# Optimization experiments

Measured on AMD Instinct MI355X. Metric: run time of the kernel, lower is better.

The kernel has to match this reference:

```python
import jax, jax.numpy as jnp
import numpy as np

D_MODEL = 128
D_STATE = 16
D_CONV = 2
EXPAND = 2
D_INNER = EXPAND * D_MODEL  # 256
DT_RANK = (D_MODEL + 15) // 16  # 8
GROUPS = 4
EPS = 1e-5


def setup_inputs() -> dict:
    key = jax.random.key(0)
    ks = jax.random.split(key, 12)
    s = lambda k, shape, sc=0.02: jax.random.normal(k, shape, dtype=jnp.float32) * sc
    inp = {
        "x_hsi": jax.random.normal(ks[0], (8, D_MODEL, 64, 64), dtype=jnp.float32),
        "W_in": s(ks[1], (D_MODEL, 2 * D_INNER)),            # in_proj (no bias)
        "conv_w": s(ks[2], (D_INNER, D_CONV), 0.5),          # depthwise causal conv, k=2
        "conv_b": s(ks[3], (D_INNER,), 0.1),
        "W_x": s(ks[4], (D_INNER, DT_RANK + 2 * D_STATE)),   # x_proj (no bias)
        "W_dt": s(ks[5], (DT_RANK, D_INNER), 0.1),
        "b_dt": s(ks[6], (D_INNER,), 0.1),
        "A_log": jnp.log(jnp.broadcast_to(jnp.arange(1, D_STATE + 1, dtype=jnp.float32), (D_INNER, D_STATE))),
        "D": jnp.ones((D_INNER,), dtype=jnp.float32),
        "W_out": s(ks[7], (D_INNER, D_MODEL)),               # out_proj (no bias)
        "gn_gamma": jnp.ones((D_MODEL,), dtype=jnp.float32),
        "gn_beta": jnp.zeros((D_MODEL,), dtype=jnp.float32),
    }
    return inp


def _causal_conv_k2(x, w, b):
    # x: [B, L, Din]; w: [Din, 2]; causal depthwise conv, kernel size 2
    xp = jnp.pad(x, ((0, 0), (1, 0), (0, 0)))
    return xp[:, :-1] * w[:, 0] + xp[:, 1:] * w[:, 1] + b


def _selective_scan(xc, dt, Bmat, Cmat, A, D):
    # xc,dt: [B,L,Din]; Bmat,Cmat: [B,L,N]; A: [Din,N]; D: [Din]
    def step(h, inp):
        dt_t, B_t, C_t, x_t = inp          # [B,Din],[B,N],[B,N],[B,Din]
        dA = jnp.exp(dt_t[..., None] * A)                      # [B,Din,N]
        dBx = dt_t[..., None] * B_t[:, None, :] * x_t[..., None]
        h = dA * h + dBx
        y = jnp.einsum('bdn,bn->bd', h, C_t)
        return h, y

    B_, L, Din = xc.shape
    h0 = jnp.zeros((B_, Din, A.shape[1]), dtype=xc.dtype)
    xs = (jnp.swapaxes(dt, 0, 1), jnp.swapaxes(Bmat, 0, 1),
          jnp.swapaxes(Cmat, 0, 1), jnp.swapaxes(xc, 0, 1))
    _, ys = jax.lax.scan(step, h0, xs)     # ys: [L,B,Din]
    return jnp.swapaxes(ys, 0, 1) + xc * D


def _mamba(x, W_in, conv_w, conv_b, W_x, W_dt, b_dt, A_log, D, W_out):
    # x: [B, L, d_model]
    xz = x @ W_in                                   # [B,L,2*Din]
    xh, z = jnp.split(xz, 2, axis=-1)
    xh = jax.nn.silu(_causal_conv_k2(xh, conv_w, conv_b))
    x_dbl = xh @ W_x                                # [B,L,dt_rank+2N]
    dt_low = x_dbl[..., :DT_RANK]
    Bmat = x_dbl[..., DT_RANK:DT_RANK + D_STATE]
    Cmat = x_dbl[..., DT_RANK + D_STATE:]
    dt = jax.nn.softplus(dt_low @ W_dt + b_dt)      # [B,L,Din]
    A = -jnp.exp(A_log)
    y = _selective_scan(xh, dt, Bmat, Cmat, A, D)
    y = y * jax.nn.silu(z)
    return y @ W_out


def _group_norm(x, gamma, beta):
    # x: [B,C,H,W]
    B_, C, H, W = x.shape
    xr = x.reshape(B_, GROUPS, -1)
    mean = xr.mean(-1, keepdims=True)
    var = xr.var(-1, keepdims=True)
    xn = ((xr - mean) * jax.lax.rsqrt(var + EPS)).reshape(B_, C, H, W)
    return xn * gamma[:, None, None] + beta[:, None, None]


def reference(x_hsi, W_in, conv_w, conv_b, W_x, W_dt, b_dt, A_log, D, W_out, gn_gamma, gn_beta):
    B_, C, H, W = x_hsi.shape
    x = jnp.transpose(x_hsi, (0, 2, 3, 1)).reshape(B_, H * W, C)
    x = _mamba(x, W_in, conv_w, conv_b, W_x, W_dt, b_dt, A_log, D, W_out)
    x = jnp.transpose(x.reshape(B_, H, W, C), (0, 3, 1, 2))
    x = jax.nn.silu(_group_norm(x, gn_gamma, gn_beta))
    return x + x_hsi
```

## Files before the change

kernel.cpp:

```cpp
#include <hip/hip_runtime.h>
#include <hip/hip_bf16.h>
#include <hip/hip_fp16.h>
#include <math.h>

#define BATCH   8
#define LSEQ    4096
#define CMODEL  128
#define DIN     256
#define NSTATE  16
#define RRANK   8
#define NCH     128
#define TCH     32

typedef __attribute__((ext_vector_type(8))) short short8;
typedef __attribute__((ext_vector_type(4))) float f32x4;
typedef __attribute__((ext_vector_type(2))) float f32x2;

__device__ __forceinline__ float sigmoid_fast(float x) {
    return __builtin_amdgcn_rcpf(1.0f + __expf(-x));
}
__device__ __forceinline__ float silu_fast(float x) { return x * sigmoid_fast(x); }
__device__ __forceinline__ float softplus_fast(float x) {
    return fmaxf(x, 0.0f) + __logf(1.0f + __expf(-fabsf(x)));
}
__device__ __forceinline__ float bf2f(unsigned short u) {
    return __uint_as_float(((unsigned)u) << 16);
}
__device__ __forceinline__ unsigned pk2bf(float a, float b) {
    __hip_bfloat162 t = __float22bfloat162_rn(make_float2(a, b));
    unsigned r;
    __builtin_memcpy(&r, &t, 4);
    return r;
}
__device__ __forceinline__ unsigned short f2bf1(float v) {
    return (unsigned short)pk2bf(v, v);
}
__device__ __forceinline__ f32x2 up2(unsigned w) {
    return (f32x2){ __uint_as_float(w << 16), __uint_as_float(w & 0xffff0000u) };
}

__device__ __forceinline__ void dA_powers2(float dtv, const float* A, bool fast,
                                           f32x2* dA2)
{
    if (fast) {
        float e1 = __expf(dtv * A[0]);
        float e2 = e1 * e1;
        dA2[0] = (f32x2){e1, e2};
        f32x2 e2s = (f32x2){e2, e2};
        #pragma unroll
        for (int j = 1; j < 8; ++j) dA2[j] = dA2[j-1] * e2s;
    } else {
        #pragma unroll
        for (int j = 0; j < 8; ++j)
            dA2[j] = (f32x2){__expf(dtv * A[2*j]), __expf(dtv * A[2*j+1])};
    }
}

#define LSTR 72

__device__ __forceinline__ void tr64_bf(const float* __restrict__ src, int lds,
                                        int r0, int c0,
                                        unsigned short* __restrict__ dst, int ldd)
{
    __shared__ float ts[64][65];
    const int tid = threadIdx.x;
    #pragma unroll
    for (int it = 0; it < 4; ++it) {
        int slot = tid + it * 256;
        int i = slot >> 4, j4 = slot & 15;
        float4 v = *(const float4*)&src[(size_t)(r0 + i) * lds + c0 + j4 * 4];
        ts[i][j4*4+0] = v.x; ts[i][j4*4+1] = v.y;
        ts[i][j4*4+2] = v.z; ts[i][j4*4+3] = v.w;
    }
    __syncthreads();
    #pragma unroll
    for (int it = 0; it < 4; ++it) {
        int slot = tid + it * 256;
        int row = slot >> 4, c4 = slot & 15;
        unsigned p0 = pk2bf(ts[c4*4+0][row], ts[c4*4+1][row]);
        unsigned p1 = pk2bf(ts[c4*4+2][row], ts[c4*4+3][row]);
        unsigned long long u = (unsigned long long)p0 | ((unsigned long long)p1 << 32);
        *(unsigned long long*)&dst[(size_t)(c0 + row) * ldd + r0 + c4 * 4] = u;
    }
}

__global__ __launch_bounds__(256) void k0_setup(
    const float* __restrict__ W_in, const float* __restrict__ W_out,
    unsigned short* __restrict__ wtin, unsigned short* __restrict__ wtout,
    float* __restrict__ part)
{
    const int bid = blockIdx.x;
    if (bid < 16) {
        int ct = bid >> 3, jt = bid & 7;
        tr64_bf(W_in, 512, ct * 64, jt * 64, wtin, 128);
    } else if (bid < 24) {
        int t3 = bid - 16;
        int kt = t3 >> 1, ct = t3 & 1;
        tr64_bf(W_out, 128, kt * 64, ct * 64, wtout, 256);
    } else {
        if (threadIdx.x < 64) part[threadIdx.x] = 0.0f;
    }
}

__global__ __launch_bounds__(512) void k1_gemm_in(
    const float* __restrict__ x_hsi, const unsigned short* __restrict__ wtin,
    unsigned short* __restrict__ xhbf, unsigned short* __restrict__ zbf)
{
    __shared__ __align__(16) unsigned short Abf[128 * LSTR];
    __shared__ __align__(16) unsigned short Bbf[256 * LSTR];
    const int tid = threadIdx.x;
    const int R0  = blockIdx.x * 128;
    const int b   = R0 >> 12;
    const int l0  = R0 & 4095;
    const int jbase = blockIdx.y * 256;

    const int w    = tid >> 6;
    const int lane = tid & 63;
    const int lm   = lane & 15;
    const int q    = lane >> 4;
    const int mbase = (w & 1) * 64;
    const int nbase = (w >> 1) * 64;

    f32x4 acc[4][4];
    #pragma unroll
    for (int i = 0; i < 4; ++i)
        #pragma unroll
        for (int j = 0; j < 4; ++j) acc[i][j] = (f32x4){0.f, 0.f, 0.f, 0.f};

    const int cq = tid & 15;
    const int lq = tid >> 4;

    for (int kc = 0; kc < 128; kc += 64) {
        __syncthreads();
        {
            float v[4][4];
            #pragma unroll
            for (int t = 0; t < 4; ++t) {
                float4 f = *(const float4*)&x_hsi[((b * 128 + kc + cq * 4 + t) << 12) + l0 + lq * 4];
                v[t][0] = f.x; v[t][1] = f.y; v[t][2] = f.z; v[t][3] = f.w;
            }
            #pragma unroll
            for (int i = 0; i < 4; ++i) {
                unsigned p0 = pk2bf(v[0][i], v[1][i]);
                unsigned p1 = pk2bf(v[2][i], v[3][i]);
                unsigned long long u = (unsigned long long)p0 | ((unsigned long long)p1 << 32);
                *(unsigned long long*)&Abf[(lq * 4 + i) * LSTR + cq * 4] = u;
            }
        }
        #pragma unroll
        for (int it = 0; it < 4; ++it) {
            int slot = tid + it * 512;
            int r = slot >> 3, seg = slot & 7;
            short8 vb = *(const short8*)&wtin[(size_t)(jbase + r) * 128 + kc + seg * 8];
            *(short8*)&Bbf[r * LSTR + seg * 8] = vb;
        }
        __syncthreads();
        #pragma unroll
        for (int kt = 0; kt < 2; ++kt) {
            short8 af[4], bfr[4];
            #pragma unroll
            for (int mt = 0; mt < 4; ++mt)
                af[mt] = *(const short8*)&Abf[(mbase + mt * 16 + lm) * LSTR + kt * 32 + q * 8];
            #pragma unroll
            for (int nt = 0; nt < 4; ++nt)
                bfr[nt] = *(const short8*)&Bbf[(nbase + nt * 16 + lm) * LSTR + kt * 32 + q * 8];
            #pragma unroll
            for (int mt = 0; mt < 4; ++mt)
                #pragma unroll
                for (int nt = 0; nt < 4; ++nt)
                    acc[mt][nt] = __builtin_amdgcn_mfma_f32_16x16x32_bf16(
                        af[mt], bfr[nt], acc[mt][nt], 0, 0, 0);
        }
    }

    const bool is_xh = (jbase == 0);
    #pragma unroll
    for (int mt = 0; mt < 4; ++mt) {
        #pragma unroll
        for (int r = 0; r < 4; ++r) {
            int row = R0 + mbase + mt * 16 + q * 4 + r;
            #pragma unroll
            for (int nt = 0; nt < 4; ++nt) {
                int col = nbase + nt * 16 + lm;
                float val = acc[mt][nt][r];
                if (is_xh) xhbf[row * 256 + col] = f2bf1(val);
                else       zbf[row * 256 + col]  = f2bf1(silu_fast(val));
            }
        }
    }
}

__global__ __launch_bounds__(256) void k4_xdbl(
    const unsigned short* __restrict__ xhbf, const float* __restrict__ conv_w,
    const float* __restrict__ conv_b, const float* __restrict__ W_x,
    float* __restrict__ xdbl, unsigned short* __restrict__ xcbf)
{
    __shared__ float xcs[128][68];
    __shared__ float wxs[64 * 40];
    __shared__ float cw0[256], cw1[256], cbs[256];
    const int tid = threadIdx.x;
    cw0[tid] = conv_w[2 * tid];
    cw1[tid] = conv_w[2 * tid + 1];
    cbs[tid] = conv_b[tid];

    const int R0 = blockIdx.x * 128;
    const int tc = tid & 7;
    const int tr = tid >> 3;

    float acc[4][5];
    #pragma unroll
    for (int i = 0; i < 4; ++i)
        #pragma unroll
        for (int j = 0; j < 5; ++j) acc[i][j] = 0.0f;

    for (int kc = 0; kc < 256; kc += 64) {
        __syncthreads();
        #pragma unroll
        for (int it = 0; it < 3; ++it) {
            int i4 = tid + it * 256;
            if (i4 < 640) ((float4*)wxs)[i4] = ((const float4*)&W_x[kc * 40])[i4];
        }
        #pragma unroll
        for (int it = 0; it < 8; ++it) {
            int idx = tid + it * 256;
            int r = idx >> 4, qq = idx & 15;
            int row = R0 + r;
            ushort4 cu = *(const ushort4*)&xhbf[(size_t)row * 256 + kc + qq * 4];
            float cur[4] = {bf2f(cu.x), bf2f(cu.y), bf2f(cu.z), bf2f(cu.w)};
            float pv[4] = {0.f, 0.f, 0.f, 0.f};
            if ((row & 4095) != 0) {
                ushort4 pu = *(const ushort4*)&xhbf[(size_t)(row - 1) * 256 + kc + qq * 4];
                pv[0] = bf2f(pu.x); pv[1] = bf2f(pu.y);
                pv[2] = bf2f(pu.z); pv[3] = bf2f(pu.w);
            }
            int d = kc + qq * 4;
            float o[4];
            #pragma unroll
            for (int e = 0; e < 4; ++e)
                o[e] = silu_fast(pv[e] * cw0[d+e] + cur[e] * cw1[d+e] + cbs[d+e]);
            *(float4*)&xcs[r][qq * 4] = make_float4(o[0], o[1], o[2], o[3]);
            unsigned p0 = pk2bf(o[0], o[1]), p1 = pk2bf(o[2], o[3]);
            unsigned long long u = (unsigned long long)p0 | ((unsigned long long)p1 << 32);
            *(unsigned long long*)&xcbf[(size_t)row * 256 + d] = u;
        }
        __syncthreads();
        #pragma unroll 2
        for (int k = 0; k < 64; ++k) {
            float wv[5];
            #pragma unroll
            for (int j = 0; j < 5; ++j) wv[j] = wxs[k * 40 + tc * 5 + j];
            #pragma unroll
            for (int i = 0; i < 4; ++i) {
                float a = xcs[tr * 4 + i][k];
                #pragma unroll
                for (int j = 0; j < 5; ++j) acc[i][j] = fmaf(a, wv[j], acc[i][j]);
            }
        }
    }
    #pragma unroll
    for (int i = 0; i < 4; ++i) {
        int row = R0 + tr * 4 + i;
        #pragma unroll
        for (int j = 0; j < 5; ++j) xdbl[row * 40 + tc * 5 + j] = acc[i][j];
    }
}

__global__ __launch_bounds__(256) void k6_scan1(
    const unsigned short* __restrict__ xcbf, const float* __restrict__ xdbl,
    const float* __restrict__ W_dt, const float* __restrict__ b_dt,
    const float* __restrict__ A_log,
    float* __restrict__ hend, float* __restrict__ dtsg,
    __half* __restrict__ dtvh)
{
    __shared__ __align__(16) unsigned char xdb[TCH * 64];
    const int d = threadIdx.x;
    const int chunk = blockIdx.x;
    const int b = blockIdx.y;
    const int t0 = b * LSEQ + chunk * TCH;

    {
        int row = d >> 3, seg = d & 7;
        const float4* src = (const float4*)&xdbl[(size_t)(t0 + row) * 40];
        if (seg < 2) {
            *(float4*)&xdb[row * 64 + seg * 16] = src[seg];
        } else if (seg < 6) {
            float4 f = src[seg];
            unsigned p0 = pk2bf(f.x, f.y), p1 = pk2bf(f.z, f.w);
            *(uint2*)&xdb[row * 64 + 32 + (seg - 2) * 8] = make_uint2(p0, p1);
        }
    }

    float A[16];
    #pragma unroll
    for (int qq = 0; qq < 4; ++qq) {
        float4 al = *(const float4*)&A_log[d * 16 + qq * 4];
        A[qq*4+0] = -__expf(al.x); A[qq*4+1] = -__expf(al.y);
        A[qq*4+2] = -__expf(al.z); A[qq*4+3] = -__expf(al.w);
    }
    bool fast = true;
    #pragma unroll
    for (int n = 1; n < 16; ++n)
        fast = fast && (fabsf(A[n] - (n + 1) * A[0]) <= 1e-4f * fabsf(A[n]) + 1e-7f);

    float wdt[8];
    #pragma unroll
    for (int r = 0; r < 8; ++r) wdt[r] = W_dt[r * 256 + d];
    const float bdt = b_dt[d];

    f32x2 h2[8];
    #pragma unroll
    for (int j = 0; j < 8; ++j) h2[j] = (f32x2){0.f, 0.f};
    float dtsum = 0.f;
    __syncthreads();

    #pragma unroll 2
    for (int tt = 0; tt < TCH; ++tt) {
        const int row = t0 + tt;
        float xcv = bf2f(xcbf[(size_t)row * 256 + d]);

        const unsigned char* xr = &xdb[tt * 64];
        float dl[8];
        *(float4*)&dl[0] = *(const float4*)xr;
        *(float4*)&dl[4] = *(const float4*)(xr + 16);
        float dtr = bdt;
        #pragma unroll
        for (int r = 0; r < 8; ++r) dtr = fmaf(dl[r], wdt[r], dtr);
        float dtv = softplus_fast(dtr);
        dtsum += dtv;
        float dtx = dtv * xcv;
        dtvh[(size_t)row * 256 + d] = __float2half(dtv);

        uint4 bu0 = *(const uint4*)(xr + 32);
        uint4 bu1 = *(const uint4*)(xr + 48);
        f32x2 Bt2[8] = {up2(bu0.x), up2(bu0.y), up2(bu0.z), up2(bu0.w),
                        up2(bu1.x), up2(bu1.y), up2(bu1.z), up2(bu1.w)};

        f32x2 dA2[8];
        dA_powers2(dtv, A, fast, dA2);
        f32x2 dtx2 = (f32x2){dtx, dtx};
        #pragma unroll
        for (int j = 0; j < 8; ++j)
            h2[j] = dA2[j] * h2[j] + dtx2 * Bt2[j];
    }

    const float* hf = (const float*)h2;
    const int base = ((b * NCH + chunk) * 256 + d) * 16;
    #pragma unroll
    for (int qq = 0; qq < 4; ++qq)
        *(float4*)&hend[base + qq * 4] = make_float4(hf[qq*4], hf[qq*4+1], hf[qq*4+2], hf[qq*4+3]);
    dtsg[(b * NCH + chunk) * 256 + d] = dtsum;
}

__global__ __launch_bounds__(256) void k7_combine(
    const float* __restrict__ dtsg, const float* __restrict__ A_log,
    float* __restrict__ hx)
{
    const int idx = blockIdx.x * 256 + threadIdx.x;
    const int b = idx >> 12;
    const int rem = idx & 4095;
    const int d = rem >> 4, n = rem & 15;
    const float An = -__expf(A_log[d * 16 + n]);
    const int base = b * NCH * 4096 + rem;
    const int sbase = b * NCH * 256 + d;
    float h = 0.f;
    float Sb[8], Eb[8];
    #pragma unroll
    for (int j = 0; j < 8; ++j) {
        Sb[j] = dtsg[sbase + j * 256];
        Eb[j] = hx[base + j * 4096];
    }
    for (int g = 0; g < NCH / 8; ++g) {
        const int o  = base + g * 32768;
        const int so = sbase + g * 2048;
        float Sn[8] = {0,0,0,0,0,0,0,0}, En[8] = {0,0,0,0,0,0,0,0};
        if (g < NCH / 8 - 1) {
            #pragma unroll
            for (int j = 0; j < 8; ++j) {
                Sn[j] = dtsg[so + 2048 + j * 256];
                En[j] = hx[o + 32768 + j * 4096];
            }
        }
        #pragma unroll
        for (int j = 0; j < 8; ++j) {
            hx[o + j * 4096] = h;
            float P = __expf(Sb[j] * An);
            h = fmaf(P, h, Eb[j]);
        }
        #pragma unroll
        for (int j = 0; j < 8; ++j) { Sb[j] = Sn[j]; Eb[j] = En[j]; }
    }
}

__global__ __launch_bounds__(256) void k8_scan2(
    const unsigned short* __restrict__ xcbf, const float* __restrict__ xdbl,
    const __half* __restrict__ dtvh, const float* __restrict__ A_log,
    const float* __restrict__ Dvec, const float* __restrict__ hin,
    const unsigned short* __restrict__ zbf, unsigned short* __restrict__ ybf)
{
    __shared__ __align__(16) unsigned char xdb[TCH * 64];
    const int d = threadIdx.x;
    const int chunk = blockIdx.x;
    const int b = blockIdx.y;
    const int t0 = b * LSEQ + chunk * TCH;

    {
        int row = d >> 3, seg = d & 7;
        float4 f = *(const float4*)&xdbl[(size_t)(t0 + row) * 40 + 8 + seg * 4];
        unsigned p0 = pk2bf(f.x, f.y), p1 = pk2bf(f.z, f.w);
        *(uint2*)&xdb[row * 64 + seg * 8] = make_uint2(p0, p1);
    }

    float A[16];
    #pragma unroll
    for (int qq = 0; qq < 4; ++qq) {
        float4 al = *(const float4*)&A_log[d * 16 + qq * 4];
        A[qq*4+0] = -__expf(al.x); A[qq*4+1] = -__expf(al.y);
        A[qq*4+2] = -__expf(al.z); A[qq*4+3] = -__expf(al.w);
    }
    bool fast = true;
    #pragma unroll
    for (int n = 1; n < 16; ++n)
        fast = fast && (fabsf(A[n] - (n + 1) * A[0]) <= 1e-4f * fabsf(A[n]) + 1e-7f);

    const float Dd = Dvec[d];

    f32x2 h2[8];
    const int hbase = ((b * NCH + chunk) * 256 + d) * 16;
    {
        float hf[16];
        #pragma unroll
        for (int qq = 0; qq < 4; ++qq) {
            float4 hv = *(const float4*)&hin[hbase + qq * 4];
            hf[qq*4+0] = hv.x; hf[qq*4+1] = hv.y; hf[qq*4+2] = hv.z; hf[qq*4+3] = hv.w;
        }
        #pragma unroll
        for (int j = 0; j < 8; ++j) h2[j] = (f32x2){hf[2*j], hf[2*j+1]};
    }
    __syncthreads();

    #pragma unroll 2
    for (int tt = 0; tt < TCH; ++tt) {
        const int row = t0 + tt;
        const size_t gi = (size_t)row * 256 + d;
        float dtv = __half2float(dtvh[gi]);
        float xcv = bf2f(xcbf[gi]);
        float dtx = dtv * xcv;

        const unsigned char* xr = &xdb[tt * 64];
        uint4 bu0 = *(const uint4*)(xr + 0);
        uint4 bu1 = *(const uint4*)(xr + 16);
        uint4 cu0 = *(const uint4*)(xr + 32);
        uint4 cu1 = *(const uint4*)(xr + 48);
        f32x2 Bt2[8] = {up2(bu0.x), up2(bu0.y), up2(bu0.z), up2(bu0.w),
                        up2(bu1.x), up2(bu1.y), up2(bu1.z), up2(bu1.w)};
        f32x2 Ct2[8] = {up2(cu0.x), up2(cu0.y), up2(cu0.z), up2(cu0.w),
                        up2(cu1.x), up2(cu1.y), up2(cu1.z), up2(cu1.w)};

        f32x2 dA2[8];
        dA_powers2(dtv, A, fast, dA2);
        f32x2 dtx2 = (f32x2){dtx, dtx};
        f32x2 yv2 = (f32x2){0.f, 0.f};
        #pragma unroll
        for (int j = 0; j < 8; ++j) {
            h2[j] = dA2[j] * h2[j] + dtx2 * Bt2[j];
            yv2 = yv2 + h2[j] * Ct2[j];
        }
        float yv = yv2.x + yv2.y;
        yv = fmaf(Dd, xcv, yv);
        ybf[gi] = f2bf1(yv * bf2f(zbf[gi]));
    }
}

__global__ __launch_bounds__(256) void k9_gemm_out(
    const unsigned short* __restrict__ ybf, const unsigned short* __restrict__ wtout,
    unsigned short* __restrict__ out_bf, float* __restrict__ part)
{
    __shared__ __align__(16) unsigned short Abf[128 * LSTR];
    __shared__ __align__(16) unsigned short Bbf[128 * LSTR];
    const int tid = threadIdx.x;
    const int R0 = blockIdx.x * 128;
    const int b  = R0 >> 12;
    const int l0 = R0 & 4095;

    const int w    = tid >> 6;
    const int lane = tid & 63;
    const int lm   = lane & 15;
    const int q    = lane >> 4;
    const int mbase = (w & 1) * 64;
    const int nbase = (w >> 1) * 64;

    f32x4 acc[4][4];
    #pragma unroll
    for (int i = 0; i < 4; ++i)
        #pragma unroll
        for (int j = 0; j < 4; ++j) acc[i][j] = (f32x4){0.f, 0.f, 0.f, 0.f};

    for (int kc = 0; kc < 256; kc += 64) {
        __syncthreads();
        #pragma unroll
        for (int it = 0; it < 4; ++it) {
            int slot = tid + it * 256;
            int r = slot >> 3, seg = slot & 7;
            short8 va = *(const short8*)&wtout[(size_t)r * 256 + kc + seg * 8];
            *(short8*)&Abf[r * LSTR + seg * 8] = va;
            short8 vb = *(const short8*)&ybf[(size_t)(R0 + r) * 256 + kc + seg * 8];
            *(short8*)&Bbf[r * LSTR + seg * 8] = vb;
        }
        __syncthreads();
        #pragma unroll
        for (int kt = 0; kt < 2; ++kt) {
            short8 af[4], bfr[4];
            #pragma unroll
            for (int mt = 0; mt < 4; ++mt)
                af[mt] = *(const short8*)&Abf[(mbase + mt * 16 + lm) * LSTR + kt * 32 + q * 8];
            #pragma unroll
            for (int nt = 0; nt < 4; ++nt)
                bfr[nt] = *(const short8*)&Bbf[(nbase + nt * 16 + lm) * LSTR + kt * 32 + q * 8];
            #pragma unroll
            for (int mt = 0; mt < 4; ++mt)
                #pragma unroll
                for (int nt = 0; nt < 4; ++nt)
                    acc[mt][nt] = __builtin_amdgcn_mfma_f32_16x16x32_bf16(
                        af[mt], bfr[nt], acc[mt][nt], 0, 0, 0);
        }
    }

    #pragma unroll
    for (int mt = 0; mt < 4; ++mt) {
        #pragma unroll
        for (int r = 0; r < 4; ++r) {
            int c = mbase + mt * 16 + q * 4 + r;
            long base = (long)(b * 128 + c) * 4096 + l0;
            #pragma unroll
            for (int nt = 0; nt < 4; ++nt)
                out_bf[base + nbase + nt * 16 + lm] = f2bf1(acc[mt][nt][r]);
        }
    }

    float s0 = 0.f, q0 = 0.f, s1 = 0.f, q1 = 0.f;
    #pragma unroll
    for (int mt = 0; mt < 4; ++mt)
        #pragma unroll
        for (int nt = 0; nt < 4; ++nt)
            #pragma unroll
            for (int r = 0; r < 4; ++r) {
                float v = acc[mt][nt][r];
                if (mt < 2) { s0 += v; q0 += v * v; }
                else        { s1 += v; q1 += v * v; }
            }
    #pragma unroll
    for (int off = 32; off > 0; off >>= 1) {
        s0 += __shfl_down(s0, off, 64);
        q0 += __shfl_down(q0, off, 64);
        s1 += __shfl_down(s1, off, 64);
        q1 += __shfl_down(q1, off, 64);
    }
    if (lane == 0) {
        int g0 = mbase >> 5;
        atomicAdd(&part[(b * 4 + g0) * 2],     s0);
        atomicAdd(&part[(b * 4 + g0) * 2 + 1], q0);
        atomicAdd(&part[(b * 4 + g0 + 1) * 2],     s1);
        atomicAdd(&part[(b * 4 + g0 + 1) * 2 + 1], q1);
    }
}

__global__ __launch_bounds__(256) void k10c_apply(
    const unsigned short* __restrict__ out_bf, const float* __restrict__ part,
    const float* __restrict__ gamma, const float* __restrict__ beta,
    const float* __restrict__ x_hsi, float* __restrict__ out)
{
    __shared__ float sstat[64];
    if (threadIdx.x < 32) {
        float S = part[threadIdx.x * 2];
        float Q = part[threadIdx.x * 2 + 1];
        const float inv_n = 1.0f / 131072.0f;
        float mean = S * inv_n;
        float var  = Q * inv_n - mean * mean;
        sstat[threadIdx.x * 2]     = mean;
        sstat[threadIdx.x * 2 + 1] = rsqrtf(var + 1e-5f);
    }
    __syncthreads();
    const int idx4 = blockIdx.x * 256 + threadIdx.x;
    const int flat = idx4 * 4;
    const int c = (flat >> 12) & 127;
    const int b = flat >> 19;
    const int g = c >> 5;
    const float mean = sstat[(b * 4 + g) * 2];
    const float inv  = sstat[(b * 4 + g) * 2 + 1];
    const float ga = gamma[c], be = beta[c];
    ushort4 u = *(const ushort4*)&out_bf[flat];
    float4 r = *(const float4*)&x_hsi[flat];
    float vv[4] = {bf2f(u.x), bf2f(u.y), bf2f(u.z), bf2f(u.w)};
    float rr[4] = {r.x, r.y, r.z, r.w};
    float o[4];
    #pragma unroll
    for (int qq = 0; qq < 4; ++qq) {
        float xn = (vv[qq] - mean) * inv;
        float gv = xn * ga + be;
        o[qq] = silu_fast(gv) + rr[qq];
    }
    *(float4*)&out[flat] = make_float4(o[0], o[1], o[2], o[3]);
}

extern "C" void kernel_launch(void* const* d_in, const int* in_sizes, int n_in,
                              void* d_out, int out_size, void* d_ws, size_t ws_size,
                              hipStream_t stream)
{
    const float* x_hsi  = (const float*)d_in[0];
    const float* W_in   = (const float*)d_in[1];
    const float* conv_w = (const float*)d_in[2];
    const float* conv_b = (const float*)d_in[3];
    const float* W_x    = (const float*)d_in[4];
    const float* W_dt   = (const float*)d_in[5];
    const float* b_dt   = (const float*)d_in[6];
    const float* A_log  = (const float*)d_in[7];
    const float* Dv     = (const float*)d_in[8];
    const float* W_out  = (const float*)d_in[9];
    const float* gnw    = (const float*)d_in[10];
    const float* gnb    = (const float*)d_in[11];

    float* ws = (float*)d_ws;
    unsigned short* xhbf = (unsigned short*)(ws + 0);
    unsigned short* zbf  = (unsigned short*)(ws + 4194304);
    float* xdbl   = ws + 8388608;
    float* hx     = ws + 8716288;
    __half* dtvh  = (__half*)(ws + 12910592);
    float* dtsg   = ws + 17104896;
    unsigned short* xcbf   = (unsigned short*)(ws + 17367040);
    unsigned short* out_bf = (unsigned short*)(ws + 21561344);
    float* part   = ws + 23658496;
    unsigned short* wtin  = (unsigned short*)(ws + 23658624);
    unsigned short* wtout = (unsigned short*)(ws + 23691392);
    unsigned short* ybf   = xhbf;
    float* outp   = (float*)d_out;

    k0_setup<<<25, 256, 0, stream>>>(W_in, W_out, wtin, wtout, part);
    k1_gemm_in<<<dim3(256, 2), 512, 0, stream>>>(x_hsi, wtin, xhbf, zbf);
    k4_xdbl<<<256, 256, 0, stream>>>(xhbf, conv_w, conv_b, W_x, xdbl, xcbf);
    k6_scan1<<<dim3(NCH, BATCH), 256, 0, stream>>>(xcbf, xdbl, W_dt, b_dt, A_log,
                                                   hx, dtsg, dtvh);
    k7_combine<<<128, 256, 0, stream>>>(dtsg, A_log, hx);
    k8_scan2<<<dim3(NCH, BATCH), 256, 0, stream>>>(xcbf, xdbl, dtvh,
                                                   A_log, Dv, hx, zbf, ybf);
    k9_gemm_out<<<256, 256, 0, stream>>>(ybf, wtout, out_bf, part);
    k10c_apply<<<4096, 256, 0, stream>>>(out_bf, part, gnw, gnb, x_hsi, outp);
}
```

Baseline: 234.6 us.

## Recompute dt in second scan pass, lengthen scan chunks, shrink xdbl and out-GEMM tiles

The second scan kernel now recomputes dt from the low-rank projection and softplus instead of reading a half-precision dt buffer that the first scan wrote, removing a large global write and read. Scan chunks double in length and halve in count. The x_proj and out_proj kernels use 64-row tiles so twice as many blocks launch. The GroupNorm partial sums are reduced in shared memory before one global atomic per group. The cost is duplicated softplus math in the second pass and longer serial chunks inside each scan block.

```diff
diff --git a/kernel.cpp b/kernel.cpp
--- a/kernel.cpp
+++ b/kernel.cpp
@@ -9,8 +9,8 @@
 #define DIN     256
 #define NSTATE  16
 #define RRANK   8
-#define NCH     128
-#define TCH     32
+#define NCH     64
+#define TCH     64
 
 typedef __attribute__((ext_vector_type(8))) short short8;
 typedef __attribute__((ext_vector_type(4))) float f32x4;
@@ -195,7 +195,7 @@
     const float* __restrict__ conv_b, const float* __restrict__ W_x,
     float* __restrict__ xdbl, unsigned short* __restrict__ xcbf)
 {
-    __shared__ float xcs[128][68];
+    __shared__ float xcs[64][68];
     __shared__ float wxs[64 * 40];
     __shared__ float cw0[256], cw1[256], cbs[256];
     const int tid = threadIdx.x;
@@ -203,13 +203,13 @@
     cw1[tid] = conv_w[2 * tid + 1];
     cbs[tid] = conv_b[tid];
 
-    const int R0 = blockIdx.x * 128;
+    const int R0 = blockIdx.x * 64;
     const int tc = tid & 7;
     const int tr = tid >> 3;
 
-    float acc[4][5];
-    #pragma unroll
-    for (int i = 0; i < 4; ++i)
+    float acc[2][5];
+    #pragma unroll
+    for (int i = 0; i < 2; ++i)
         #pragma unroll
         for (int j = 0; j < 5; ++j) acc[i][j] = 0.0f;
 
@@ -221,7 +221,7 @@
             if (i4 < 640) ((float4*)wxs)[i4] = ((const float4*)&W_x[kc * 40])[i4];
         }
         #pragma unroll
-        for (int it = 0; it < 8; ++it) {
+        for (int it = 0; it < 4; ++it) {
             int idx = tid + it * 256;
             int r = idx >> 4, qq = idx & 15;
             int row = R0 + r;
@@ -250,16 +250,16 @@
             #pragma unroll
             for (int j = 0; j < 5; ++j) wv[j] = wxs[k * 40 + tc * 5 + j];
             #pragma unroll
-            for (int i = 0; i < 4; ++i) {
-                float a = xcs[tr * 4 + i][k];
+            for (int i = 0; i < 2; ++i) {
+                float a = xcs[tr * 2 + i][k];
                 #pragma unroll
                 for (int j = 0; j < 5; ++j) acc[i][j] = fmaf(a, wv[j], acc[i][j]);
             }
         }
     }
     #pragma unroll
-    for (int i = 0; i < 4; ++i) {
-        int row = R0 + tr * 4 + i;
+    for (int i = 0; i < 2; ++i) {
+        int row = R0 + tr * 2 + i;
         #pragma unroll
         for (int j = 0; j < 5; ++j) xdbl[row * 40 + tc * 5 + j] = acc[i][j];
     }
@@ -269,8 +269,7 @@
     const unsigned short* __restrict__ xcbf, const float* __restrict__ xdbl,
     const float* __restrict__ W_dt, const float* __restrict__ b_dt,
     const float* __restrict__ A_log,
-    float* __restrict__ hend, float* __restrict__ dtsg,
-    __half* __restrict__ dtvh)
+    float* __restrict__ hend, float* __restrict__ dtsg)
 {
     __shared__ __align__(16) unsigned char xdb[TCH * 64];
     const int d = threadIdx.x;
@@ -278,8 +277,10 @@
     const int b = blockIdx.y;
     const int t0 = b * LSEQ + chunk * TCH;
 
-    {
-        int row = d >> 3, seg = d & 7;
+    #pragma unroll
+    for (int it = 0; it < 2; ++it) {
+        int slot = d + it * 256;
+        int row = slot >> 3, seg = slot & 7;
         const float4* src = (const float4*)&xdbl[(size_t)(t0 + row) * 40];
         if (seg < 2) {
             *(float4*)&xdb[row * 64 + seg * 16] = src[seg];
@@ -328,7 +329,6 @@
         float dtv = softplus_fast(dtr);
         dtsum += dtv;
         float dtx = dtv * xcv;
-        dtvh[(size_t)row * 256 + d] = __float2half(dtv);
 
         uint4 bu0 = *(const uint4*)(xr + 32);
         uint4 bu1 = *(const uint4*)(xr + 48);
@@ -393,21 +393,29 @@
 
 __global__ __launch_bounds__(256) void k8_scan2(
     const unsigned short* __restrict__ xcbf, const float* __restrict__ xdbl,
-    const __half* __restrict__ dtvh, const float* __restrict__ A_log,
+    const float* __restrict__ W_dt, const float* __restrict__ b_dt,
+    const float* __restrict__ A_log,
     const float* __restrict__ Dvec, const float* __restrict__ hin,
     const unsigned short* __restrict__ zbf, unsigned short* __restrict__ ybf)
 {
-    __shared__ __align__(16) unsigned char xdb[TCH * 64];
+    __shared__ __align__(16) unsigned char xdb[TCH * 96];
     const int d = threadIdx.x;
     const int chunk = blockIdx.x;
     const int b = blockIdx.y;
     const int t0 = b * LSEQ + chunk * TCH;
 
-    {
-        int row = d >> 3, seg = d & 7;
-        float4 f = *(const float4*)&xdbl[(size_t)(t0 + row) * 40 + 8 + seg * 4];
+    #pragma unroll
+    for (int it = 0; it < 2; ++it) {
+        int slot = d + it * 256;
+        int row = slot >> 3, s8 = slot & 7;
+        float4 f = *(const float4*)&xdbl[(size_t)(t0 + row) * 40 + 8 + s8 * 4];
         unsigned p0 = pk2bf(f.x, f.y), p1 = pk2bf(f.z, f.w);
-        *(uint2*)&xdb[row * 64 + seg * 8] = make_uint2(p0, p1);
+        *(uint2*)&xdb[row * 96 + 32 + s8 * 8] = make_uint2(p0, p1);
+    }
+    if (d < 128) {
+        int row = d >> 1, seg = d & 1;
+        *(float4*)&xdb[row * 96 + seg * 16] =
+            *(const float4*)&xdbl[(size_t)(t0 + row) * 40 + seg * 4];
     }
 
     float A[16];
@@ -422,6 +430,10 @@
     for (int n = 1; n < 16; ++n)
         fast = fast && (fabsf(A[n] - (n + 1) * A[0]) <= 1e-4f * fabsf(A[n]) + 1e-7f);
 
+    float wdt[8];
+    #pragma unroll
+    for (int r = 0; r < 8; ++r) wdt[r] = W_dt[r * 256 + d];
+    const float bdt = b_dt[d];
     const float Dd = Dvec[d];
 
     f32x2 h2[8];
@@ -442,15 +454,22 @@
     for (int tt = 0; tt < TCH; ++tt) {
         const int row = t0 + tt;
         const size_t gi = (size_t)row * 256 + d;
-        float dtv = __half2float(dtvh[gi]);
         float xcv = bf2f(xcbf[gi]);
+
+        const unsigned char* xr = &xdb[tt * 96];
+        float dl[8];
+        *(float4*)&dl[0] = *(const float4*)xr;
+        *(float4*)&dl[4] = *(const float4*)(xr + 16);
+        float dtr = bdt;
+        #pragma unroll
+        for (int r = 0; r < 8; ++r) dtr = fmaf(dl[r], wdt[r], dtr);
+        float dtv = softplus_fast(dtr);
         float dtx = dtv * xcv;
 
-        const unsigned char* xr = &xdb[tt * 64];
-        uint4 bu0 = *(const uint4*)(xr + 0);
-        uint4 bu1 = *(const uint4*)(xr + 16);
-        uint4 cu0 = *(const uint4*)(xr + 32);
-        uint4 cu1 = *(const uint4*)(xr + 48);
+        uint4 bu0 = *(const uint4*)(xr + 32);
+        uint4 bu1 = *(const uint4*)(xr + 48);
+        uint4 cu0 = *(const uint4*)(xr + 64);
+        uint4 cu1 = *(const uint4*)(xr + 80);
         f32x2 Bt2[8] = {up2(bu0.x), up2(bu0.y), up2(bu0.z), up2(bu0.w),
                         up2(bu1.x), up2(bu1.y), up2(bu1.z), up2(bu1.w)};
         f32x2 Ct2[8] = {up2(cu0.x), up2(cu0.y), up2(cu0.z), up2(cu0.w),
@@ -476,9 +495,10 @@
     unsigned short* __restrict__ out_bf, float* __restrict__ part)
 {
     __shared__ __align__(16) unsigned short Abf[128 * LSTR];
-    __shared__ __align__(16) unsigned short Bbf[128 * LSTR];
+    __shared__ __align__(16) unsigned short Bbf[64 * LSTR];
+    __shared__ float pred[8];
     const int tid = threadIdx.x;
-    const int R0 = blockIdx.x * 128;
+    const int R0 = blockIdx.x * 64;
     const int b  = R0 >> 12;
     const int l0 = R0 & 4095;
 
@@ -487,13 +507,15 @@
     const int lm   = lane & 15;
     const int q    = lane >> 4;
     const int mbase = (w & 1) * 64;
-    const int nbase = (w >> 1) * 64;
-
-    f32x4 acc[4][4];
+    const int nbase = (w >> 1) * 32;
+
+    if (tid < 8) pred[tid] = 0.0f;
+
+    f32x4 acc[4][2];
     #pragma unroll
     for (int i = 0; i < 4; ++i)
         #pragma unroll
-        for (int j = 0; j < 4; ++j) acc[i][j] = (f32x4){0.f, 0.f, 0.f, 0.f};
+        for (int j = 0; j < 2; ++j) acc[i][j] = (f32x4){0.f, 0.f, 0.f, 0.f};
 
     for (int kc = 0; kc < 256; kc += 64) {
         __syncthreads();
@@ -503,23 +525,28 @@
             int r = slot >> 3, seg = slot & 7;
             short8 va = *(const short8*)&wtout[(size_t)r * 256 + kc + seg * 8];
             *(short8*)&Abf[r * LSTR + seg * 8] = va;
+        }
+        #pragma unroll
+        for (int it = 0; it < 2; ++it) {
+            int slot = tid + it * 256;
+            int r = slot >> 3, seg = slot & 7;
             short8 vb = *(const short8*)&ybf[(size_t)(R0 + r) * 256 + kc + seg * 8];
             *(short8*)&Bbf[r * LSTR + seg * 8] = vb;
         }
         __syncthreads();
         #pragma unroll
         for (int kt = 0; kt < 2; ++kt) {
-            short8 af[4], bfr[4];
+            short8 af[4], bfr[2];
             #pragma unroll
             for (int mt = 0; mt < 4; ++mt)
                 af[mt] = *(const short8*)&Abf[(mbase + mt * 16 + lm) * LSTR + kt * 32 + q * 8];
             #pragma unroll
-            for (int nt = 0; nt < 4; ++nt)
+            for (int nt = 0; nt < 2; ++nt)
                 bfr[nt] = *(const short8*)&Bbf[(nbase + nt * 16 + lm) * LSTR + kt * 32 + q * 8];
             #pragma unroll
             for (int mt = 0; mt < 4; ++mt)
                 #pragma unroll
-                for (int nt = 0; nt < 4; ++nt)
+                for (int nt = 0; nt < 2; ++nt)
                     acc[mt][nt] = __builtin_amdgcn_mfma_f32_16x16x32_bf16(
                         af[mt], bfr[nt], acc[mt][nt], 0, 0, 0);
         }
@@ -532,7 +559,7 @@
             int c = mbase + mt * 16 + q * 4 + r;
             long base = (long)(b * 128 + c) * 4096 + l0;
             #pragma unroll
-            for (int nt = 0; nt < 4; ++nt)
+            for (int nt = 0; nt < 2; ++nt)
                 out_bf[base + nbase + nt * 16 + lm] = f2bf1(acc[mt][nt][r]);
         }
     }
@@ -541,7 +568,7 @@
     #pragma unroll
     for (int mt = 0; mt < 4; ++mt)
         #pragma unroll
-        for (int nt = 0; nt < 4; ++nt)
+        for (int nt = 0; nt < 2; ++nt)
             #pragma unroll
             for (int r = 0; r < 4; ++r) {
                 float v = acc[mt][nt][r];
@@ -557,11 +584,13 @@
     }
     if (lane == 0) {
         int g0 = mbase >> 5;
-        atomicAdd(&part[(b * 4 + g0) * 2],     s0);
-        atomicAdd(&part[(b * 4 + g0) * 2 + 1], q0);
-        atomicAdd(&part[(b * 4 + g0 + 1) * 2],     s1);
-        atomicAdd(&part[(b * 4 + g0 + 1) * 2 + 1], q1);
-    }
+        atomicAdd(&pred[g0 * 2],           s0);
+        atomicAdd(&pred[g0 * 2 + 1],       q0);
+        atomicAdd(&pred[(g0 + 1) * 2],     s1);
+        atomicAdd(&pred[(g0 + 1) * 2 + 1], q1);
+    }
+    __syncthreads();
+    if (tid < 8) atomicAdd(&part[b * 8 + tid], pred[tid]);
 }
 
 __global__ __launch_bounds__(256) void k10c_apply(
@@ -624,24 +653,23 @@
     unsigned short* zbf  = (unsigned short*)(ws + 4194304);
     float* xdbl   = ws + 8388608;
     float* hx     = ws + 8716288;
-    __half* dtvh  = (__half*)(ws + 12910592);
-    float* dtsg   = ws + 17104896;
-    unsigned short* xcbf   = (unsigned short*)(ws + 17367040);
-    unsigned short* out_bf = (unsigned short*)(ws + 21561344);
-    float* part   = ws + 23658496;
-    unsigned short* wtin  = (unsigned short*)(ws + 23658624);
-    unsigned short* wtout = (unsigned short*)(ws + 23691392);
+    float* dtsg   = ws + 10813440;
+    unsigned short* xcbf   = (unsigned short*)(ws + 10944512);
+    unsigned short* out_bf = (unsigned short*)(ws + 15138816);
+    float* part   = ws + 17235968;
+    unsigned short* wtin  = (unsigned short*)(ws + 17236032);
+    unsigned short* wtout = (unsigned short*)(ws + 17268800);
     unsigned short* ybf   = xhbf;
     float* outp   = (float*)d_out;
 
     k0_setup<<<25, 256, 0, stream>>>(W_in, W_out, wtin, wtout, part);
     k1_gemm_in<<<dim3(256, 2), 512, 0, stream>>>(x_hsi, wtin, xhbf, zbf);
-    k4_xdbl<<<256, 256, 0, stream>>>(xhbf, conv_w, conv_b, W_x, xdbl, xcbf);
+    k4_xdbl<<<512, 256, 0, stream>>>(xhbf, conv_w, conv_b, W_x, xdbl, xcbf);
     k6_scan1<<<dim3(NCH, BATCH), 256, 0, stream>>>(xcbf, xdbl, W_dt, b_dt, A_log,
-                                                   hx, dtsg, dtvh);
+                                                   hx, dtsg);
     k7_combine<<<128, 256, 0, stream>>>(dtsg, A_log, hx);
-    k8_scan2<<<dim3(NCH, BATCH), 256, 0, stream>>>(xcbf, xdbl, dtvh,
-                                                   A_log, Dv, hx, zbf, ybf);
-    k9_gemm_out<<<256, 256, 0, stream>>>(ybf, wtout, out_bf, part);
+    k8_scan2<<<dim3(NCH, BATCH), 256, 0, stream>>>(xcbf, xdbl, W_dt, b_dt, A_log,
+                                                   Dv, hx, zbf, ybf);
+    k9_gemm_out<<<512, 256, 0, stream>>>(ybf, wtout, out_bf, part);
     k10c_apply<<<4096, 256, 0, stream>>>(out_bf, part, gnw, gnb, x_hsi, outp);
 }
```

Result: faster. 215.3 us (-8.2%).
